# Performance work log

Hardware: AMD Instinct MI355X
Metric: run time of the kernel (lower is better)

## Reference

```python
import jax, jax.numpy as jnp
import numpy as np

B, S, D, H = 1, 4096, 768, 12
HD = D // H
FF = 4 * D
EPS = 1e-5


def _layer_norm(x, w, b):
    mu = jnp.mean(x, axis=-1, keepdims=True)
    var = jnp.mean((x - mu) ** 2, axis=-1, keepdims=True)
    return (x - mu) * jax.lax.rsqrt(var + EPS) * w + b


def setup_inputs() -> dict:
    key = jax.random.key(0)
    ks = jax.random.split(key, 16)
    s = 0.02
    inp = {
        "hidden_states": jax.random.normal(ks[0], (B, S, D), jnp.float32),
        "attention_mask": jnp.ones((B, S), jnp.int32),
        "ln1_w": jnp.ones((D,), jnp.float32),
        "ln1_b": jnp.zeros((D,), jnp.float32),
        "wq": jax.random.normal(ks[1], (D, D), jnp.float32) * s,
        "bq": jnp.zeros((D,), jnp.float32),
        "wk": jax.random.normal(ks[2], (D, D), jnp.float32) * s,
        "bk": jnp.zeros((D,), jnp.float32),
        "wv": jax.random.normal(ks[3], (D, D), jnp.float32) * s,
        "bv": jnp.zeros((D,), jnp.float32),
        "wo": jax.random.normal(ks[4], (D, D), jnp.float32) * s,
        "bo": jnp.zeros((D,), jnp.float32),
        "ln2_w": jnp.ones((D,), jnp.float32),
        "ln2_b": jnp.zeros((D,), jnp.float32),
        "w_up": jax.random.normal(ks[5], (D, FF), jnp.float32) * s,
        "b_up": jnp.zeros((FF,), jnp.float32),
        "w_down": jax.random.normal(ks[6], (FF, D), jnp.float32) * s,
        "b_down": jnp.zeros((D,), jnp.float32),
    }
    return inp


def reference(hidden_states, attention_mask, ln1_w, ln1_b, wq, bq, wk, bk, wv, bv,
              wo, bo, ln2_w, ln2_b, w_up, b_up, w_down, b_down):
    b, s, _ = hidden_states.shape
    residual = hidden_states
    x = _layer_norm(hidden_states, ln1_w, ln1_b)
    # projections; weights stored [in, out]
    q = (x @ wq + bq).reshape(b, s, H, HD).transpose(0, 2, 1, 3)  # (b,h,s,hd)
    k = (x @ wk + bk).reshape(b, s, H, HD).transpose(0, 2, 1, 3)
    v = (x @ wv + bv).reshape(b, s, H, HD).transpose(0, 2, 1, 3)
    scores = jnp.einsum("bhqd,bhkd->bhqk", q, k) / np.float32(np.sqrt(HD))
    causal = jnp.triu(jnp.ones((s, s), bool), k=1)  # True above diagonal -> mask
    neg_inf = jnp.float32(-jnp.inf)
    scores = jnp.where(causal[None, None, :, :], neg_inf, scores)
    pad = (attention_mask[:, None, None, :] == 0)
    scores = jnp.where(pad, neg_inf, scores)
    weights = jax.nn.softmax(scores, axis=-1)
    attn = jnp.einsum("bhqk,bhkd->bhqd", weights, v)
    attn = attn.transpose(0, 2, 1, 3).reshape(b, s, D)
    hidden = residual + (attn @ wo + bo)
    # FFN
    residual = hidden
    y = _layer_norm(hidden, ln2_w, ln2_b)
    y = jax.nn.gelu(y @ w_up + b_up, approximate=False)
    y = y @ w_down + b_down
    return residual + y
```

## Files before the change

### kernel.cpp

```cpp
#include <hip/hip_runtime.h>
#include <cstdint>
#include <cstddef>


#define S_  4096
#define D_  768
#define H_  12
#define HD_ 64
#define FF_ 3072
#define SD_ (4096 * 768)

typedef short  short8  __attribute__((ext_vector_type(8)));
typedef float  floatx4 __attribute__((ext_vector_type(4)));

__device__ __forceinline__ float bf2f(unsigned short h) {
  union { unsigned int u; float f; } v; v.u = ((unsigned int)h) << 16; return v.f;
}
__device__ __forceinline__ unsigned short f2bf(float f) {
  union { unsigned int u; float f; } v; v.f = f;
  unsigned int u = v.u;
  return (unsigned short)((u + 0x7FFFu + ((u >> 16) & 1u)) >> 16);
}
__device__ __forceinline__ unsigned short f2bf_fast(float f) {
  union { unsigned int u; float f; } v; v.f = f;
  return (unsigned short)((v.u + 0x8000u) >> 16);
}
__device__ __forceinline__ void gload_lds16(const unsigned short* g, unsigned short* l) {
  __builtin_amdgcn_global_load_lds(
      (const __attribute__((address_space(1))) unsigned int*)g,
      (__attribute__((address_space(3))) unsigned int*)l, 16, 0, 0);
}

__global__ void k_cvt_f32(const void* __restrict__ src, float* __restrict__ dst,
                          int n, const int* __restrict__ flagp) {
  const int flag = *flagp;
  for (int i = blockIdx.x * blockDim.x + threadIdx.x; i < n; i += gridDim.x * blockDim.x)
    dst[i] = flag ? ((const float*)src)[i] : bf2f(((const unsigned short*)src)[i]);
}

__global__ __launch_bounds__(256) void k_cvt_t6(
    const void* s0, const void* s1, const void* s2, const void* s3,
    const void* s4, const void* s5,
    unsigned short* d0, unsigned short* d1, unsigned short* d2,
    unsigned short* d3, unsigned short* d4, unsigned short* d5,
    const int* __restrict__ flagp) {
  __shared__ unsigned short T[64 * 65];
  const int flag = *flagp;
  const int b = blockIdx.x;
  const void* src; unsigned short* dst; int K, N, ti;
  if (b < 576) {
    const int seg = b / 144; ti = b - seg * 144; K = 768; N = 768;
    const void* ss[4] = {s0, s1, s2, s3};
    unsigned short* dd[4] = {d0, d1, d2, d3};
    src = ss[seg]; dst = dd[seg];
  } else if (b < 1152) { ti = b - 576;  K = 768;  N = 3072; src = s4; dst = d4; }
  else                 { ti = b - 1152; K = 3072; N = 768;  src = s5; dst = d5; }
  const int nx = N >> 6;
  const int n0 = (ti % nx) * 64, k0 = (ti / nx) * 64;
  const int t = threadIdx.x;
  const int cl = t & 63, rg = t >> 6;
#pragma unroll
  for (int i = 0; i < 16; ++i) {
    const int kl = rg * 16 + i;
    const size_t si = (size_t)(k0 + kl) * N + n0 + cl;
    T[kl * 65 + cl] = flag ? f2bf(((const float*)src)[si]) : ((const unsigned short*)src)[si];
  }
  __syncthreads();
#pragma unroll
  for (int i = 0; i < 16; ++i) {
    const int nl = rg * 16 + i;
    dst[(size_t)(n0 + nl) * K + k0 + cl] = T[cl * 65 + nl];
  }
}

__global__ void k_cvt_params(const void* p0, const void* p1, const void* p2, const void* p3,
                             const void* p4, const void* p5, const void* p6, const void* p7,
                             const void* p8, const void* p9,
                             float* __restrict__ dst, int* __restrict__ flagp) {
  const int flag = (((const unsigned int*)p0)[0] == 0x3F800000u) ? 1 : 0;
  int i = blockIdx.x * 256 + threadIdx.x;
  if (i == 0) *flagp = flag;
  if (i >= 9984) return;
  const void* src; int j;
  if (i < 6912) {
    int seg = i / 768; j = i - seg * 768;
    const void* tbl[9] = {p0, p1, p2, p3, p4, p5, p6, p7, p8};
    src = tbl[seg];
  } else { src = p9; j = i - 6912; }
  dst[i] = flag ? ((const float*)src)[j] : bf2f(((const unsigned short*)src)[j]);
}

__global__ __launch_bounds__(256) void k_ln(const float* __restrict__ x,
                                            const float* __restrict__ w,
                                            const float* __restrict__ b,
                                            unsigned short* __restrict__ out) {
  const int row = blockIdx.x, t = threadIdx.x;
  const float* xr = x + (size_t)row * D_;
  float v0 = xr[t], v1 = xr[t + 256], v2 = xr[t + 512];
  float s = v0 + v1 + v2;
  float ss = v0 * v0 + v1 * v1 + v2 * v2;
  for (int off = 32; off > 0; off >>= 1) {
    s  += __shfl_down(s, off);
    ss += __shfl_down(ss, off);
  }
  __shared__ float sb[4], ssb[4];
  const int wid = t >> 6, lane = t & 63;
  if (lane == 0) { sb[wid] = s; ssb[wid] = ss; }
  __syncthreads();
  s  = sb[0] + sb[1] + sb[2] + sb[3];
  ss = ssb[0] + ssb[1] + ssb[2] + ssb[3];
  const float mu   = s * (1.0f / D_);
  const float var  = ss * (1.0f / D_) - mu * mu;
  const float rstd = rsqrtf(var + 1e-5f);
  unsigned short* orow = out + (size_t)row * D_;
  orow[t]       = f2bf((v0 - mu) * rstd * w[t]       + b[t]);
  orow[t + 256] = f2bf((v1 - mu) * rstd * w[t + 256] + b[t + 256]);
  orow[t + 512] = f2bf((v2 - mu) * rstd * w[t + 512] + b[t + 512]);
}

template <int TBM, int TBN>
__global__ __launch_bounds__(256) void k_gemm_t(
    const unsigned short* __restrict__ A, const unsigned short* __restrict__ Wt,
    const float* __restrict__ bias, const float* __restrict__ resid,
    void* __restrict__ Cout, int M, int N, int K, int mode, const int* __restrict__ flagp) {
  constexpr int MI = TBM / 32, MJ = TBN / 32;
  __shared__ __align__(16) unsigned short As[TBM * 32];
  __shared__ __align__(16) unsigned short Bs[TBN * 32];
  const int t = threadIdx.x;
  const int w = t >> 6, lane = t & 63;
  const int quad = lane >> 4, l16 = lane & 15;
  const int mb = blockIdx.y * TBM, nb = blockIdx.x * TBN;
  const int wm = (w >> 1) * (TBM / 2), wn = (w & 1) * (TBN / 2);
  const int grow = lane >> 2;
  const int gcol = (lane & 3) * 8;

  floatx4 acc[MI][MJ];
#pragma unroll
  for (int i = 0; i < MI; ++i)
#pragma unroll
    for (int j = 0; j < MJ; ++j) acc[i][j] = (floatx4){0.f, 0.f, 0.f, 0.f};

  for (int k0 = 0; k0 < K; k0 += 32) {
    __syncthreads();
#pragma unroll
    for (int r = 0; r < TBM / 64; ++r) {
      const int ch = r * 4 + w;
      gload_lds16(A + (size_t)(mb + ch * 16 + grow) * K + k0 + gcol, &As[ch * 512]);
    }
#pragma unroll
    for (int r = 0; r < TBN / 64; ++r) {
      const int ch = r * 4 + w;
      gload_lds16(Wt + (size_t)(nb + ch * 16 + grow) * K + k0 + gcol, &Bs[ch * 512]);
    }
    __syncthreads();

    union { short8 v; uint4 q; } fa[MI], fb[MJ];
#pragma unroll
    for (int i = 0; i < MI; ++i)
      fa[i].q = *(const uint4*)&As[(wm + i * 16 + l16) * 32 + quad * 8];
#pragma unroll
    for (int j = 0; j < MJ; ++j)
      fb[j].q = *(const uint4*)&Bs[(wn + j * 16 + l16) * 32 + quad * 8];
#pragma unroll
    for (int i = 0; i < MI; ++i)
#pragma unroll
      for (int j = 0; j < MJ; ++j)
        acc[i][j] = __builtin_amdgcn_mfma_f32_16x16x32_bf16(fa[i].v, fb[j].v, acc[i][j], 0, 0, 0);
  }

  const int flag = (mode == 3) ? *flagp : 0;
#pragma unroll
  for (int i = 0; i < MI; ++i) {
#pragma unroll
    for (int j = 0; j < MJ; ++j) {
      const int col = nb + wn + j * 16 + l16;
      const float bv = bias[col];
#pragma unroll
      for (int r = 0; r < 4; ++r) {
        const int row = mb + wm + i * 16 + quad * 4 + r;
        const size_t idx = (size_t)row * N + col;
        float v = acc[i][j][r] + bv;
        if (mode == 0) {
          ((unsigned short*)Cout)[idx] = f2bf(v);
        } else if (mode == 1) {
          ((float*)Cout)[idx] = v + resid[idx];
        } else if (mode == 2) {
          float g = 0.5f * v * (1.0f + erff(v * 0.70710678118f));
          ((unsigned short*)Cout)[idx] = f2bf(g);
        } else if (mode == 5) {
          unsigned short* q = (unsigned short*)Cout;
          if (col < 768)        q[(size_t)row * 768 + col] = f2bf(v);
          else if (col < 1536) (q + SD_)[(size_t)row * 768 + col - 768] = f2bf(v);
          else                 (q + 2 * (size_t)SD_)[(size_t)(col - 1536) * 4096 + row] = f2bf(v);
        } else {
          v += resid[idx];
          if (flag) ((float*)Cout)[idx] = v;
          else      ((unsigned short*)Cout)[idx] = f2bf(v);
        }
      }
    }
  }
}

#define LK 72
__global__ __launch_bounds__(256) void k_attn_chunk(
    const unsigned short* __restrict__ qb, const unsigned short* __restrict__ kb,
    const unsigned short* __restrict__ vtb, const int* __restrict__ amask,
    unsigned short* __restrict__ Opart, float* __restrict__ Lpart) {
  const int h = blockIdx.y, x = blockIdx.x;
  int g, base;
  if (x < 8)       { g = 0; base = 0; }
  else if (x < 24) { g = 1; base = 8; }
  else if (x < 48) { g = 2; base = 24; }
  else             { g = 3; base = 48; }
  const int rem = x - base;
  const int qt = 8 * g + rem / (g + 1);
  const int c  = rem % (g + 1);
  const int qbase = qt * 128;
  const int kt0 = c * 16;
  const int kt1 = min(kt0 + 16, 2 * qt + 2);

  __shared__ __align__(16) unsigned short Kt[64 * LK];
  __shared__ __align__(16) unsigned short Vt[64 * LK];
  __shared__ __align__(16) unsigned short Ps[128 * LK];
  __shared__ int Mk[64];
  const int t = threadIdx.x;
  const int w = t >> 6, lane = t & 63;
  const int quad = lane >> 4, l16 = lane & 15;
  const int sr = t >> 2, sc = (t & 3) * 16;

  union { short8 v; uint4 q; } qf[2][2];
#pragma unroll
  for (int sub = 0; sub < 2; ++sub) {
    const unsigned short* qp =
        qb + (size_t)(qbase + w * 32 + sub * 16 + l16) * D_ + h * HD_ + quad * 8;
    qf[sub][0].q = *(const uint4*)qp;
    qf[sub][1].q = *(const uint4*)(qp + 32);
  }
  short8 onesB;
#pragma unroll
  for (int e = 0; e < 8; ++e) onesB[e] = (short)0x3F80;
  unsigned short* myP = &Ps[w * 32 * LK];

  floatx4 O[2][4], Lacc[2];
#pragma unroll
  for (int sub = 0; sub < 2; ++sub) {
    Lacc[sub] = (floatx4){0.f, 0.f, 0.f, 0.f};
#pragma unroll
    for (int dc = 0; dc < 4; ++dc) O[sub][dc] = (floatx4){0.f, 0.f, 0.f, 0.f};
  }
  const float sscale = 0.125f * 1.4426950408889634f;
  const int qrow0 = qbase + w * 32 + quad * 4;

  for (int kt = kt0; kt < kt1; ++kt) {
    const int kbase = kt * 64;
    __syncthreads();
    {
      const unsigned short* ks = kb + (size_t)(kbase + sr) * D_ + h * HD_ + sc;
      *(uint4*)&Kt[sr * LK + sc]     = *(const uint4*)ks;
      *(uint4*)&Kt[sr * LK + sc + 8] = *(const uint4*)(ks + 8);
      const unsigned short* vs = vtb + (size_t)(h * HD_ + sr) * S_ + kbase + sc;
      *(uint4*)&Vt[sr * LK + sc]     = *(const uint4*)vs;
      *(uint4*)&Vt[sr * LK + sc + 8] = *(const uint4*)(vs + 8);
      if (t < 64) Mk[t] = amask[kbase + t];
    }
    __syncthreads();

    const bool diag = (kt >= 2 * qt);
#pragma unroll
    for (int kc = 0; kc < 4; ++kc) {
      union { short8 v; uint4 q; } kf[2];
      const unsigned short* p0 = &Kt[(kc * 16 + l16) * LK + quad * 8];
      kf[0].q = *(const uint4*)p0;
      kf[1].q = *(const uint4*)(p0 + 32);
      floatx4 cc[2];
#pragma unroll
      for (int sub = 0; sub < 2; ++sub) {
        cc[sub] = (floatx4){0.f, 0.f, 0.f, 0.f};
        cc[sub] = __builtin_amdgcn_mfma_f32_16x16x32_bf16(qf[sub][0].v, kf[0].v, cc[sub], 0, 0, 0);
        cc[sub] = __builtin_amdgcn_mfma_f32_16x16x32_bf16(qf[sub][1].v, kf[1].v, cc[sub], 0, 0, 0);
      }
      const float mb = (Mk[kc * 16 + l16] == 0) ? -127.f : 0.f;
      const int kg = kbase + kc * 16 + l16;
#pragma unroll
      for (int sub = 0; sub < 2; ++sub)
#pragma unroll
        for (int r = 0; r < 4; ++r) {
          float sv = cc[sub][r] * sscale + mb;
          if (diag && kg > qrow0 + sub * 16 + r) sv = -127.f;
          myP[(sub * 16 + quad * 4 + r) * LK + kc * 16 + l16] = f2bf_fast(exp2f(sv));
        }
    }
    union { short8 v; uint4 q; } pf[2][2];
#pragma unroll
    for (int sub = 0; sub < 2; ++sub) {
      const unsigned short* p0 = &myP[(sub * 16 + l16) * LK + quad * 8];
      pf[sub][0].q = *(const uint4*)p0;
      pf[sub][1].q = *(const uint4*)(p0 + 32);
      Lacc[sub] = __builtin_amdgcn_mfma_f32_16x16x32_bf16(pf[sub][0].v, onesB, Lacc[sub], 0, 0, 0);
      Lacc[sub] = __builtin_amdgcn_mfma_f32_16x16x32_bf16(pf[sub][1].v, onesB, Lacc[sub], 0, 0, 0);
    }
#pragma unroll
    for (int dc = 0; dc < 4; ++dc) {
      union { short8 v; uint4 q; } vf[2];
      const unsigned short* p0 = &Vt[(dc * 16 + l16) * LK + quad * 8];
      vf[0].q = *(const uint4*)p0;
      vf[1].q = *(const uint4*)(p0 + 32);
#pragma unroll
      for (int sub = 0; sub < 2; ++sub) {
        O[sub][dc] = __builtin_amdgcn_mfma_f32_16x16x32_bf16(pf[sub][0].v, vf[0].v, O[sub][dc], 0, 0, 0);
        O[sub][dc] = __builtin_amdgcn_mfma_f32_16x16x32_bf16(pf[sub][1].v, vf[1].v, O[sub][dc], 0, 0, 0);
      }
    }
  }

  const size_t slot = (size_t)h * 80 + x;
#pragma unroll
  for (int sub = 0; sub < 2; ++sub) {
#pragma unroll
    for (int dc = 0; dc < 4; ++dc)
#pragma unroll
      for (int r = 0; r < 4; ++r)
        Opart[slot * 8192 + (w * 32 + sub * 16 + quad * 4 + r) * 64 + dc * 16 + l16] =
            f2bf(O[sub][dc][r]);
    if (l16 == 0) {
#pragma unroll
      for (int r = 0; r < 4; ++r)
        Lpart[slot * 128 + w * 32 + sub * 16 + quad * 4 + r] = Lacc[sub][r];
    }
  }
}

__global__ __launch_bounds__(256) void k_attn_merge(
    const unsigned short* __restrict__ Opart, const float* __restrict__ Lpart,
    unsigned short* __restrict__ ob) {
  const int qt = blockIdx.x, h = blockIdx.y;
  const int t = threadIdx.x;
  const int row = t >> 1, half = (t & 1) * 32;
  const int g = qt >> 3;
  const int nch = g + 1;
  const int cb = h * 80 + 4 * g * (g + 1) + (qt & 7) * (g + 1);
  float L = 0.f;
  float acc[32];
#pragma unroll
  for (int j = 0; j < 32; ++j) acc[j] = 0.f;
  for (int ci = 0; ci < nch; ++ci) {
    L += Lpart[(size_t)(cb + ci) * 128 + row];
    const unsigned short* op = Opart + (size_t)(cb + ci) * 8192 + row * 64 + half;
#pragma unroll
    for (int j4 = 0; j4 < 4; ++j4) {
      union { uint4 v; unsigned short e[8]; } u;
      u.v = *(const uint4*)(op + j4 * 8);
#pragma unroll
      for (int e = 0; e < 8; ++e) acc[j4 * 8 + e] += bf2f(u.e[e]);
    }
  }
  const float inv = 1.f / L;
  unsigned short* orow = ob + (size_t)(qt * 128 + row) * D_ + h * HD_ + half;
#pragma unroll
  for (int j4 = 0; j4 < 4; ++j4) {
    union { uint4 v; unsigned short e[8]; } u;
#pragma unroll
    for (int e = 0; e < 8; ++e) u.e[e] = f2bf(acc[j4 * 8 + e] * inv);
    *(uint4*)(orow + j4 * 8) = u.v;
  }
}

extern "C" void kernel_launch(void* const* d_in, const int* in_sizes, int n_in,
                              void* d_out, int out_size, void* d_ws, size_t ws_size,
                              hipStream_t stream) {
  const void* hidden = d_in[0];
  const int*  amask  = (const int*)d_in[1];
  const void* ln1w = d_in[2];  const void* ln1b = d_in[3];
  const void* wq   = d_in[4];  const void* bq   = d_in[5];
  const void* wk   = d_in[6];  const void* bk   = d_in[7];
  const void* wv   = d_in[8];  const void* bv   = d_in[9];
  const void* wo   = d_in[10]; const void* bo   = d_in[11];
  const void* ln2w = d_in[12]; const void* ln2b = d_in[13];
  const void* wup  = d_in[14]; const void* bup  = d_in[15];
  const void* wdn  = d_in[16]; const void* bdn  = d_in[17];

  char* ws = (char*)d_ws;
  size_t off = 0;
  auto alloc = [&](size_t bytes) {
    char* p = ws + off;
    off += (bytes + 255) & ~(size_t)255;
    return p;
  };
  const size_t SD = (size_t)SD_;
  int*            flagp = (int*)alloc(4);
  float*          h1    = (float*)alloc(SD * 4);
  float*          prm   = (float*)alloc(9984 * 4);
  float*          h2    = (float*)alloc(SD * 4);
  unsigned short* xb    = (unsigned short*)alloc(SD * 2);
  unsigned short* wqkvt = (unsigned short*)alloc((size_t)2304 * 768 * 2);
  unsigned short* wot   = (unsigned short*)alloc((size_t)768 * 768 * 2);
  unsigned short* wupt  = (unsigned short*)alloc((size_t)3072 * 768 * 2);
  unsigned short* wdnt  = (unsigned short*)alloc((size_t)768 * 3072 * 2);
  unsigned short* big   = (unsigned short*)alloc((size_t)S_ * FF_ * 2);
  unsigned short* qb2 = big;
  unsigned short* kb2 = big + SD;
  unsigned short* vtb = big + 2 * SD;
  unsigned short* ab  = big + 3 * SD;
  unsigned short* ffb = big;
  unsigned short* Opart = (unsigned short*)h2;
  float*          Lpart = (float*)((char*)h2 + (size_t)960 * 8192 * 2);

  float* f_ln1w = prm;        float* f_ln1b = prm + 768;
  float* f_ln2w = prm + 1536; float* f_ln2b = prm + 2304;
  float* f_bqkv = prm + 3072; float* f_bo = prm + 5376;
  float* f_bdn = prm + 6144;  float* f_bup = prm + 6912;

  k_cvt_params<<<39, 256, 0, stream>>>(ln1w, ln1b, ln2w, ln2b, bq, bk, bv, bo, bdn, bup,
                                       prm, flagp);
  k_cvt_f32<<<1024, 256, 0, stream>>>(hidden, h1, (int)SD, flagp);
  k_cvt_t6<<<1728, 256, 0, stream>>>(wq, wk, wv, wo, wup, wdn,
                                     wqkvt, wqkvt + 768 * 768, wqkvt + 2 * 768 * 768,
                                     wot, wupt, wdnt, flagp);

  k_ln<<<S_, 256, 0, stream>>>(h1, f_ln1w, f_ln1b, xb);

  k_gemm_t<128, 128><<<dim3(18, 32), 256, 0, stream>>>(
      xb, wqkvt, f_bqkv, nullptr, qb2, S_, 2304, 768, 5, flagp);

  k_attn_chunk<<<dim3(80, 12), 256, 0, stream>>>(qb2, kb2, vtb, amask, Opart, Lpart);
  k_attn_merge<<<dim3(32, 12), 256, 0, stream>>>(Opart, Lpart, ab);

  k_gemm_t<128, 64><<<dim3(12, 32), 256, 0, stream>>>(
      ab, wot, f_bo, h1, h2, S_, 768, 768, 1, flagp);

  k_ln<<<S_, 256, 0, stream>>>(h2, f_ln2w, f_ln2b, xb);

  k_gemm_t<128, 128><<<dim3(24, 32), 256, 0, stream>>>(
      xb, wupt, f_bup, nullptr, ffb, S_, 3072, 768, 2, flagp);
  k_gemm_t<128, 64><<<dim3(12, 32), 256, 0, stream>>>(
      ffb, wdnt, f_bdn, h2, d_out, S_, 768, 3072, 3, flagp);
}
```

Measured before the change: 406.0 us.

## Split-K the FFN down-projection into three partial GEMMs plus a merge kernel

```diff
diff --git a/kernel.cpp b/kernel.cpp
--- a/kernel.cpp
+++ b/kernel.cpp
@@ -122,7 +122,8 @@
 __global__ __launch_bounds__(256) void k_gemm_t(
     const unsigned short* __restrict__ A, const unsigned short* __restrict__ Wt,
     const float* __restrict__ bias, const float* __restrict__ resid,
-    void* __restrict__ Cout, int M, int N, int K, int mode, const int* __restrict__ flagp) {
+    void* __restrict__ Cout, void* __restrict__ aux,
+    int M, int N, int K, int Ks, int mode, const int* __restrict__ flagp) {
   constexpr int MI = TBM / 32, MJ = TBN / 32;
   __shared__ __align__(16) unsigned short As[TBM * 32];
   __shared__ __align__(16) unsigned short Bs[TBN * 32];
@@ -130,6 +131,7 @@
   const int w = t >> 6, lane = t & 63;
   const int quad = lane >> 4, l16 = lane & 15;
   const int mb = blockIdx.y * TBM, nb = blockIdx.x * TBN;
+  const int kb = blockIdx.z * K;
   const int wm = (w >> 1) * (TBM / 2), wn = (w & 1) * (TBN / 2);
   const int grow = lane >> 2;
   const int gcol = (lane & 3) * 8;
@@ -145,12 +147,12 @@
 #pragma unroll
     for (int r = 0; r < TBM / 64; ++r) {
       const int ch = r * 4 + w;
-      gload_lds16(A + (size_t)(mb + ch * 16 + grow) * K + k0 + gcol, &As[ch * 512]);
+      gload_lds16(A + (size_t)(mb + ch * 16 + grow) * Ks + kb + k0 + gcol, &As[ch * 512]);
     }
 #pragma unroll
     for (int r = 0; r < TBN / 64; ++r) {
       const int ch = r * 4 + w;
-      gload_lds16(Wt + (size_t)(nb + ch * 16 + grow) * K + k0 + gcol, &Bs[ch * 512]);
+      gload_lds16(Wt + (size_t)(nb + ch * 16 + grow) * Ks + kb + k0 + gcol, &Bs[ch * 512]);
     }
     __syncthreads();
 
@@ -174,7 +176,7 @@
 #pragma unroll
     for (int j = 0; j < MJ; ++j) {
       const int col = nb + wn + j * 16 + l16;
-      const float bv = bias[col];
+      const float bv = (mode == 6) ? 0.f : bias[col];
 #pragma unroll
       for (int r = 0; r < 4; ++r) {
         const int row = mb + wm + i * 16 + quad * 4 + r;
@@ -192,12 +194,41 @@
           if (col < 768)        q[(size_t)row * 768 + col] = f2bf(v);
           else if (col < 1536) (q + SD_)[(size_t)row * 768 + col - 768] = f2bf(v);
           else                 (q + 2 * (size_t)SD_)[(size_t)(col - 1536) * 4096 + row] = f2bf(v);
+        } else if (mode == 6) {
+          unsigned short* P = (blockIdx.z == 2)
+              ? (unsigned short*)aux
+              : (unsigned short*)Cout + (size_t)blockIdx.z * SD_;
+          P[idx] = f2bf(v);
         } else {
           v += resid[idx];
           if (flag) ((float*)Cout)[idx] = v;
           else      ((unsigned short*)Cout)[idx] = f2bf(v);
         }
       }
+    }
+  }
+}
+
+__global__ __launch_bounds__(256) void k_dn_merge(
+    const unsigned short* __restrict__ p01, const unsigned short* __restrict__ p2,
+    const float* __restrict__ bias, const float* __restrict__ resid,
+    void* __restrict__ out, const int* __restrict__ flagp) {
+  const int flag = *flagp;
+  const size_t i0 = ((size_t)blockIdx.x * 256 + threadIdx.x) * 16;
+#pragma unroll
+  for (int g = 0; g < 2; ++g) {
+    const size_t base = i0 + g * 8;
+    union { uint4 v; unsigned short e[8]; } ua, ub, uc;
+    ua.v = *(const uint4*)(p01 + base);
+    ub.v = *(const uint4*)(p01 + SD_ + base);
+    uc.v = *(const uint4*)(p2 + base);
+    const int col = (int)(base % D_);
+#pragma unroll
+    for (int e = 0; e < 8; ++e) {
+      const float s = bf2f(ua.e[e]) + bf2f(ub.e[e]) + bf2f(uc.e[e])
+                    + bias[col + e] + resid[base + e];
+      if (flag) ((float*)out)[base + e] = s;
+      else      ((unsigned short*)out)[base + e] = f2bf(s);
     }
   }
 }
@@ -405,6 +436,8 @@
   unsigned short* ffb = big;
   unsigned short* Opart = (unsigned short*)h2;
   float*          Lpart = (float*)((char*)h2 + (size_t)960 * 8192 * 2);
+  unsigned short* dnp01 = (unsigned short*)h1;
+  unsigned short* dnp2  = xb;
 
   float* f_ln1w = prm;        float* f_ln1b = prm + 768;
   float* f_ln2w = prm + 1536; float* f_ln2b = prm + 2304;
@@ -421,18 +454,20 @@
   k_ln<<<S_, 256, 0, stream>>>(h1, f_ln1w, f_ln1b, xb);
 
   k_gemm_t<128, 128><<<dim3(18, 32), 256, 0, stream>>>(
-      xb, wqkvt, f_bqkv, nullptr, qb2, S_, 2304, 768, 5, flagp);
+      xb, wqkvt, f_bqkv, nullptr, qb2, nullptr, S_, 2304, 768, 768, 5, flagp);
 
   k_attn_chunk<<<dim3(80, 12), 256, 0, stream>>>(qb2, kb2, vtb, amask, Opart, Lpart);
   k_attn_merge<<<dim3(32, 12), 256, 0, stream>>>(Opart, Lpart, ab);
 
   k_gemm_t<128, 64><<<dim3(12, 32), 256, 0, stream>>>(
-      ab, wot, f_bo, h1, h2, S_, 768, 768, 1, flagp);
+      ab, wot, f_bo, h1, h2, nullptr, S_, 768, 768, 768, 1, flagp);
 
   k_ln<<<S_, 256, 0, stream>>>(h2, f_ln2w, f_ln2b, xb);
 
   k_gemm_t<128, 128><<<dim3(24, 32), 256, 0, stream>>>(
-      xb, wupt, f_bup, nullptr, ffb, S_, 3072, 768, 2, flagp);
-  k_gemm_t<128, 64><<<dim3(12, 32), 256, 0, stream>>>(
-      ffb, wdnt, f_bdn, h2, d_out, S_, 768, 3072, 3, flagp);
-}
+      xb, wupt, f_bup, nullptr, ffb, nullptr, S_, 3072, 768, 768, 2, flagp);
+
+  k_gemm_t<128, 64><<<dim3(12, 32, 3), 256, 0, stream>>>(
+      ffb, wdnt, f_bdn, nullptr, dnp01, dnp2, S_, 768, 1024, 3072, 6, flagp);
+  k_dn_merge<<<768, 256, 0, stream>>>(dnp01, dnp2, f_bdn, h2, d_out, flagp);
+}
```

Result: slower. 421.9 us (+3.9%).
